# Performance work log

Hardware: AMD Instinct MI355X
Metric: run time of the kernel (lower is better)

The kernel has to match this reference:

```python
import jax, jax.numpy as jnp
import numpy as np

B, C, L = 8, 256, 2048
D = C // 8  # q/k channel dim = 32


def setup_inputs() -> dict:
    key = jax.random.key(0)
    kx, kq, kk, kv, kg = jax.random.split(key, 5)
    kq1, kq2 = jax.random.split(kq)
    kk1, kk2 = jax.random.split(kk)
    kv1, kv2 = jax.random.split(kv)
    s = 0.05
    return {
        "x": jax.random.normal(kx, (B, C, L), dtype=jnp.float32),
        "Wq": jax.random.normal(kq1, (D, C), dtype=jnp.float32) * s,
        "bq": jax.random.normal(kq2, (D,), dtype=jnp.float32) * s,
        "Wk": jax.random.normal(kk1, (D, C), dtype=jnp.float32) * s,
        "bk": jax.random.normal(kk2, (D,), dtype=jnp.float32) * s,
        "Wv": jax.random.normal(kv1, (C, C), dtype=jnp.float32) * s,
        "bv": jax.random.normal(kv2, (C,), dtype=jnp.float32) * s,
        "gamma": jax.random.normal(kg, (1,), dtype=jnp.float32) * 0.1,
    }


def reference(x, Wq, bq, Wk, bk, Wv, bv, gamma):
    # 1x1 Conv1d == per-position channel matmul
    Q = jnp.einsum("dc,bcl->bld", Wq, x) + bq            # (B, L, D)
    K = jnp.einsum("dc,bcl->bdl", Wk, x) + bk[:, None]   # (B, D, L)
    V = jnp.einsum("oc,bcl->bol", Wv, x) + bv[:, None]   # (B, C, L)
    scale = jnp.float32(1.0 / np.sqrt(D))
    # attn[b, i, j]: softmax over j (keys)
    attn = jax.nn.softmax(jnp.einsum("bid,bdj->bij", Q, K) * scale, axis=-1)
    # out = V @ attn^T : out[b, c, i] = sum_j V[b, c, j] * attn[b, i, j]
    out = jnp.einsum("bcj,bij->bci", V, attn)            # (B, C, L)
    return gamma * out + x
```

## Files before the change

### kernel.cpp

```cpp
#include <hip/hip_runtime.h>
#include <stdint.h>


#define BB 8
#define CC 256
#define LL 2048
#define DD 32

typedef unsigned short u16;
typedef __attribute__((ext_vector_type(8))) short short8;
typedef __attribute__((ext_vector_type(4))) float f32x4;

#define SCALE_LOG2E 0.2550348612f

static __device__ __forceinline__ uint32_t pack2bf16(float hi, float lo) {
    return (__float_as_uint(hi) & 0xFFFF0000u) | (__float_as_uint(lo) >> 16);
}

static __device__ __forceinline__ float fexp2(float v) {
#if __has_builtin(__builtin_amdgcn_exp2f)
    return __builtin_amdgcn_exp2f(v);
#else
    return exp2f(v);
#endif
}

static __device__ __forceinline__ float frcp(float v) {
#if __has_builtin(__builtin_amdgcn_rcpf)
    return __builtin_amdgcn_rcpf(v);
#else
    return 1.0f / v;
#endif
}

__global__ __launch_bounds__(256) void prep_w_kernel(
    const float* __restrict__ Wq, const float* __restrict__ Wk,
    const float* __restrict__ Wv, u16* __restrict__ Wh)
{
    int idx = blockIdx.x * 256 + threadIdx.x;
    int r = idx >> 6;
    int c4 = (idx & 63) << 2;
    const float* src;
    if (r < 32)       src = Wq + (size_t)r * CC + c4;
    else if (r < 64)  src = Wk + (size_t)(r - 32) * CC + c4;
    else              src = Wv + (size_t)(r - 64) * CC + c4;
    float4 v = *(const float4*)src;
    uint2 o;
    o.x = pack2bf16(v.y, v.x);
    o.y = pack2bf16(v.w, v.z);
    *(uint2*)(Wh + (size_t)r * CC + c4) = o;
}

__global__ __launch_bounds__(512, 2) void proj_kernel(
    const float* __restrict__ x, const u16* __restrict__ Wh,
    const float* __restrict__ bq, const float* __restrict__ bk,
    const float* __restrict__ bv,
    u16* __restrict__ Qh, u16* __restrict__ Kth, u16* __restrict__ Vh)
{
    __shared__ u16 xls[32 * 264];
    const int blk = blockIdx.x;
    const int b = blk & 7;
    const int l0 = (blk >> 3) << 5;
    const int tid = threadIdx.x;
    const int w = tid >> 6;
    const int lane = tid & 63;
    const int ln = lane & 15;
    const int q = lane >> 4;

#pragma unroll
    for (int cc = 0; cc < 4; ++cc) {
        const int c = cc * 64 + (tid >> 3);
        const int l4 = (tid & 7) * 4;
        const float4 v = *(const float4*)(x + ((size_t)(b * CC + c)) * LL + l0 + l4);
        xls[(l4 + 0) * 264 + c] = (u16)(__float_as_uint(v.x) >> 16);
        xls[(l4 + 1) * 264 + c] = (u16)(__float_as_uint(v.y) >> 16);
        xls[(l4 + 2) * 264 + c] = (u16)(__float_as_uint(v.z) >> 16);
        xls[(l4 + 3) * 264 + c] = (u16)(__float_as_uint(v.w) >> 16);
    }
    __syncthreads();

    const int wl = w & 1;
    const int wm = w >> 1;
    const int mbase = wm * 80;
    const int l = l0 + wl * 16 + ln;

    f32x4 acc[5];
#pragma unroll
    for (int i = 0; i < 5; ++i) acc[i] = (f32x4){0.f, 0.f, 0.f, 0.f};

#pragma unroll
    for (int c0 = 0; c0 < CC; c0 += 32) {
        const short8 bf = *(const short8*)(&xls[(wl * 16 + ln) * 264 + c0 + q * 8]);
#pragma unroll
        for (int mt = 0; mt < 5; ++mt) {
            const short8 af = *(const short8*)(Wh + (size_t)(mbase + mt * 16 + ln) * CC + c0 + q * 8);
            acc[mt] = __builtin_amdgcn_mfma_f32_16x16x32_bf16(af, bf, acc[mt], 0, 0, 0);
        }
    }

#pragma unroll
    for (int mt = 0; mt < 5; ++mt) {
        const int rg = mbase + mt * 16 + q * 4;
        if (rg < 32) {
            float v0 = (acc[mt][0] + bq[rg + 0]) * SCALE_LOG2E;
            float v1 = (acc[mt][1] + bq[rg + 1]) * SCALE_LOG2E;
            float v2 = (acc[mt][2] + bq[rg + 2]) * SCALE_LOG2E;
            float v3 = (acc[mt][3] + bq[rg + 3]) * SCALE_LOG2E;
            uint2 o; o.x = pack2bf16(v1, v0); o.y = pack2bf16(v3, v2);
            *(uint2*)(Qh + ((size_t)(b * LL) + l) * DD + rg) = o;
        } else if (rg < 64) {
            const int rk = rg - 32;
            float v0 = acc[mt][0] + bk[rk + 0];
            float v1 = acc[mt][1] + bk[rk + 1];
            float v2 = acc[mt][2] + bk[rk + 2];
            float v3 = acc[mt][3] + bk[rk + 3];
            uint2 o; o.x = pack2bf16(v1, v0); o.y = pack2bf16(v3, v2);
            *(uint2*)(Kth + ((size_t)(b * LL) + l) * DD + rk) = o;
        } else {
            const int cv = rg - 64;
#pragma unroll
            for (int rr = 0; rr < 4; ++rr) {
                const float v = acc[mt][rr] + bv[cv + rr];
                Vh[((size_t)(b * CC) + cv + rr) * LL + l] = (u16)(__float_as_uint(v) >> 16);
            }
        }
    }
}

#define PJ 136

__global__ __launch_bounds__(512, 4) void attn_kernel(
    const u16* __restrict__ Qh, const u16* __restrict__ Kth,
    const u16* __restrict__ Vh, const float* __restrict__ x,
    const float* __restrict__ gamma, float* __restrict__ out)
{
    __shared__ __attribute__((aligned(16))) u16 pbuf[2][32][PJ];
    __shared__ float lbuf[8][32];

    const int blk = blockIdx.x;
    const int b = blk & 7;
    const int i0 = (blk >> 3) << 5;
    const int tid = threadIdx.x;
    const int w = tid >> 6;
    const int lane = tid & 63;
    const int ln = lane & 15;
    const int q = lane >> 4;

    const u16* Qb = Qh + ((size_t)(b * LL) + i0) * DD;
    const u16* Kb = Kth + ((size_t)(b * LL) + w * 16 + ln) * DD + q * 8;
    const u16* Vb = Vh + ((size_t)(b * CC) + w * 32) * LL;

    short8 qf[2];
#pragma unroll
    for (int it = 0; it < 2; ++it)
        qf[it] = *(const short8*)(Qb + (size_t)(it * 16 + ln) * DD + q * 8);

    const f32x4 zf = {0.f, 0.f, 0.f, 0.f};
    f32x4 oacc[2][2];
#pragma unroll
    for (int a = 0; a < 2; ++a)
#pragma unroll
        for (int c = 0; c < 2; ++c) oacc[a][c] = zf;
    float lsum[2] = {0.f, 0.f};

    short8 kf = *(const short8*)(Kb);

    for (int n = 0; n < 16; ++n) {
        const int jb = n * 128;

        short8 vf[2][4];
#pragma unroll
        for (int ct = 0; ct < 2; ++ct)
#pragma unroll
            for (int kk = 0; kk < 4; ++kk)
                vf[ct][kk] = *(const short8*)(Vb + (size_t)(ct * 16 + ln) * LL + jb + kk * 32 + q * 8);
        const short8 kn = *(const short8*)(Kb + (size_t)((n < 15 ? n + 1 : n) * 128) * DD);

        u16* ps = &pbuf[n & 1][0][0];
#pragma unroll
        for (int it = 0; it < 2; ++it) {
            const f32x4 st = __builtin_amdgcn_mfma_f32_16x16x32_bf16(kf, qf[it], zf, 0, 0, 0);
            const float e0 = fexp2(st[0]), e1 = fexp2(st[1]);
            const float e2 = fexp2(st[2]), e3 = fexp2(st[3]);
            lsum[it] += (e0 + e1) + (e2 + e3);
            uint2 d; d.x = pack2bf16(e1, e0); d.y = pack2bf16(e3, e2);
            *(uint2*)(&ps[(it * 16 + ln) * PJ + w * 16 + q * 4]) = d;
        }
        __syncthreads();

        __builtin_amdgcn_s_setprio(1);
#pragma unroll
        for (int kk = 0; kk < 4; ++kk) {
            const short8 pf0 = *(const short8*)(&ps[(size_t)ln * PJ + kk * 32 + q * 8]);
            const short8 pf1 = *(const short8*)(&ps[(size_t)(16 + ln) * PJ + kk * 32 + q * 8]);
#pragma unroll
            for (int ct = 0; ct < 2; ++ct) {
                oacc[ct][0] = __builtin_amdgcn_mfma_f32_16x16x32_bf16(vf[ct][kk], pf0, oacc[ct][0], 0, 0, 0);
                oacc[ct][1] = __builtin_amdgcn_mfma_f32_16x16x32_bf16(vf[ct][kk], pf1, oacc[ct][1], 0, 0, 0);
            }
        }
        __builtin_amdgcn_s_setprio(0);
        kf = kn;
    }

#pragma unroll
    for (int it = 0; it < 2; ++it) {
        float s = lsum[it];
        s += __shfl_xor(s, 16);
        s += __shfl_xor(s, 32);
        lsum[it] = s;
    }
    if (q == 0) {
        lbuf[w][ln] = lsum[0];
        lbuf[w][16 + ln] = lsum[1];
    }
    __syncthreads();

    float linv[2];
#pragma unroll
    for (int it = 0; it < 2; ++it) {
        float s = 0.f;
#pragma unroll
        for (int w8 = 0; w8 < 8; ++w8) s += lbuf[w8][it * 16 + ln];
        linv[it] = frcp(s);
    }

    const float g = gamma[0];
#pragma unroll
    for (int ct = 0; ct < 2; ++ct)
#pragma unroll
        for (int it = 0; it < 2; ++it) {
#pragma unroll
            for (int r = 0; r < 4; ++r) {
                const int c = w * 32 + ct * 16 + q * 4 + r;
                const size_t idx = ((size_t)(b * CC + c)) * LL + i0 + it * 16 + ln;
                out[idx] = g * (oacc[ct][it][r] * linv[it]) + x[idx];
            }
        }
}

extern "C" void kernel_launch(void* const* d_in, const int* in_sizes, int n_in,
                              void* d_out, int out_size, void* d_ws, size_t ws_size,
                              hipStream_t stream)
{
    const float* x     = (const float*)d_in[0];
    const float* Wq    = (const float*)d_in[1];
    const float* bq    = (const float*)d_in[2];
    const float* Wk    = (const float*)d_in[3];
    const float* bk    = (const float*)d_in[4];
    const float* Wv    = (const float*)d_in[5];
    const float* bv    = (const float*)d_in[6];
    const float* gamma = (const float*)d_in[7];
    float* out = (float*)d_out;

    uint8_t* ws = (uint8_t*)d_ws;
    u16* Wh  = (u16*)(ws + 0x000000);
    u16* Qh  = (u16*)(ws + 0x040000);
    u16* Kth = (u16*)(ws + 0x140000);
    u16* Vh  = (u16*)(ws + 0x240000);

    prep_w_kernel<<<80, 256, 0, stream>>>(Wq, Wk, Wv, Wh);
    proj_kernel<<<512, 512, 0, stream>>>(x, Wh, bq, bk, bv, Qh, Kth, Vh);
    attn_kernel<<<512, 512, 0, stream>>>(Qh, Kth, Vh, x, gamma, out);
}
```

Baseline: 171.0 us.

## Restructure attention tiling per-wave query rows with channel split; stage V stores

The attention kernel is retiled so each block covers 256 query rows and 64 value channels. Each wave owns 32 query rows and computes its own full score rows, which removes the cross-wave P exchange and the row-sum reduction through shared memory. This trades the 8-wave shared softmax tile for recomputing QK^T four times, once per channel group, and halves the grid to 256 blocks with launch bounds of one block per CU. Separately, the projection kernel stages V in LDS so it can be written to global memory with coalesced 16-byte stores instead of scattered 2-byte stores.

```diff
diff --git a/kernel.cpp b/kernel.cpp
--- a/kernel.cpp
+++ b/kernel.cpp
@@ -58,6 +58,7 @@
     u16* __restrict__ Qh, u16* __restrict__ Kth, u16* __restrict__ Vh)
 {
     __shared__ u16 xls[32 * 264];
+    __shared__ __attribute__((aligned(16))) u16 vls[256 * 40];
     const int blk = blockIdx.x;
     const int b = blk & 7;
     const int l0 = (blk >> 3) << 5;
@@ -83,6 +84,7 @@
     const int wm = w >> 1;
     const int mbase = wm * 80;
     const int l = l0 + wl * 16 + ln;
+    const int li = wl * 16 + ln;
 
     f32x4 acc[5];
 #pragma unroll
@@ -121,34 +123,45 @@
 #pragma unroll
             for (int rr = 0; rr < 4; ++rr) {
                 const float v = acc[mt][rr] + bv[cv + rr];
-                Vh[((size_t)(b * CC) + cv + rr) * LL + l] = (u16)(__float_as_uint(v) >> 16);
+                vls[(cv + rr) * 40 + li] = (u16)(__float_as_uint(v) >> 16);
             }
         }
     }
-}
-
-#define PJ 136
-
-__global__ __launch_bounds__(512, 4) void attn_kernel(
+
+    __syncthreads();
+    {
+        const int row = tid >> 1;
+        const int h = (tid & 1) * 16;
+        const u16* src = &vls[row * 40 + h];
+        const uint4 v0 = *(const uint4*)(src);
+        const uint4 v1 = *(const uint4*)(src + 8);
+        uint4* dst = (uint4*)(Vh + ((size_t)(b * CC) + row) * LL + l0 + h);
+        dst[0] = v0;
+        dst[1] = v1;
+    }
+}
+
+__global__ __launch_bounds__(512, 1) void attn_kernel(
     const u16* __restrict__ Qh, const u16* __restrict__ Kth,
     const u16* __restrict__ Vh, const float* __restrict__ x,
     const float* __restrict__ gamma, float* __restrict__ out)
 {
-    __shared__ __attribute__((aligned(16))) u16 pbuf[2][32][PJ];
-    __shared__ float lbuf[8][32];
+    __shared__ __attribute__((aligned(16))) u16 Plds[256][72];
 
     const int blk = blockIdx.x;
-    const int b = blk & 7;
-    const int i0 = (blk >> 3) << 5;
+    const int b  = blk & 7;
+    const int c0 = ((blk >> 3) & 3) << 6;
+    const int i0 = (blk >> 5) << 8;
     const int tid = threadIdx.x;
     const int w = tid >> 6;
     const int lane = tid & 63;
     const int ln = lane & 15;
     const int q = lane >> 4;
 
-    const u16* Qb = Qh + ((size_t)(b * LL) + i0) * DD;
-    const u16* Kb = Kth + ((size_t)(b * LL) + w * 16 + ln) * DD + q * 8;
-    const u16* Vb = Vh + ((size_t)(b * CC) + w * 32) * LL;
+    u16* pb = &Plds[w * 32][0];
+    const u16* Qb = Qh + ((size_t)(b * LL) + i0 + w * 32) * DD;
+    const u16* Kb = Kth + (size_t)(b * LL) * DD;
+    const u16* Vb = Vh + ((size_t)(b * CC) + c0) * LL;
 
     short8 qf[2];
 #pragma unroll
@@ -156,87 +169,86 @@
         qf[it] = *(const short8*)(Qb + (size_t)(it * 16 + ln) * DD + q * 8);
 
     const f32x4 zf = {0.f, 0.f, 0.f, 0.f};
-    f32x4 oacc[2][2];
-#pragma unroll
-    for (int a = 0; a < 2; ++a)
+    f32x4 oacc[4][2];
+#pragma unroll
+    for (int a = 0; a < 4; ++a)
 #pragma unroll
         for (int c = 0; c < 2; ++c) oacc[a][c] = zf;
     float lsum[2] = {0.f, 0.f};
 
-    short8 kf = *(const short8*)(Kb);
-
-    for (int n = 0; n < 16; ++n) {
-        const int jb = n * 128;
-
-        short8 vf[2][4];
-#pragma unroll
-        for (int ct = 0; ct < 2; ++ct)
-#pragma unroll
-            for (int kk = 0; kk < 4; ++kk)
-                vf[ct][kk] = *(const short8*)(Vb + (size_t)(ct * 16 + ln) * LL + jb + kk * 32 + q * 8);
-        const short8 kn = *(const short8*)(Kb + (size_t)((n < 15 ? n + 1 : n) * 128) * DD);
-
-        u16* ps = &pbuf[n & 1][0][0];
-#pragma unroll
-        for (int it = 0; it < 2; ++it) {
-            const f32x4 st = __builtin_amdgcn_mfma_f32_16x16x32_bf16(kf, qf[it], zf, 0, 0, 0);
-            const float e0 = fexp2(st[0]), e1 = fexp2(st[1]);
-            const float e2 = fexp2(st[2]), e3 = fexp2(st[3]);
-            lsum[it] += (e0 + e1) + (e2 + e3);
-            uint2 d; d.x = pack2bf16(e1, e0); d.y = pack2bf16(e3, e2);
-            *(uint2*)(&ps[(it * 16 + ln) * PJ + w * 16 + q * 4]) = d;
-        }
+    short8 kf[4];
+#pragma unroll
+    for (int jt = 0; jt < 4; ++jt)
+        kf[jt] = *(const short8*)(Kb + (size_t)(jt * 16 + ln) * DD + q * 8);
+
+    for (int n = 0; n < 32; ++n) {
+        const int jb = n * 64;
+        const int jbn = (n < 31) ? jb + 64 : jb;
+
+        short8 vf[4][2];
+#pragma unroll
+        for (int ct = 0; ct < 4; ++ct)
+#pragma unroll
+            for (int jk = 0; jk < 2; ++jk)
+                vf[ct][jk] = *(const short8*)(Vb + (size_t)(ct * 16 + ln) * LL + jb + jk * 32 + q * 8);
+        short8 kn[4];
+#pragma unroll
+        for (int jt = 0; jt < 4; ++jt)
+            kn[jt] = *(const short8*)(Kb + (size_t)(jbn + jt * 16 + ln) * DD + q * 8);
+
+#pragma unroll
+        for (int jt = 0; jt < 4; ++jt) {
+#pragma unroll
+            for (int it = 0; it < 2; ++it) {
+                const f32x4 st = __builtin_amdgcn_mfma_f32_16x16x32_bf16(kf[jt], qf[it], zf, 0, 0, 0);
+                const float e0 = fexp2(st[0]), e1 = fexp2(st[1]);
+                const float e2 = fexp2(st[2]), e3 = fexp2(st[3]);
+                lsum[it] += (e0 + e1) + (e2 + e3);
+                uint2 d; d.x = pack2bf16(e1, e0); d.y = pack2bf16(e3, e2);
+                *(uint2*)(&pb[(it * 16 + ln) * 72 + jt * 16 + q * 4]) = d;
+            }
+        }
+
+#pragma unroll
+        for (int jk = 0; jk < 2; ++jk) {
+            short8 pf[2];
+#pragma unroll
+            for (int it = 0; it < 2; ++it)
+                pf[it] = *(const short8*)(&pb[(it * 16 + ln) * 72 + jk * 32 + q * 8]);
+#pragma unroll
+            for (int ct = 0; ct < 4; ++ct)
+#pragma unroll
+                for (int it = 0; it < 2; ++it)
+                    oacc[ct][it] = __builtin_amdgcn_mfma_f32_16x16x32_bf16(
+                        vf[ct][jk], pf[it], oacc[ct][it], 0, 0, 0);
+        }
+
+#pragma unroll
+        for (int jt = 0; jt < 4; ++jt) kf[jt] = kn[jt];
+
         __syncthreads();
-
-        __builtin_amdgcn_s_setprio(1);
-#pragma unroll
-        for (int kk = 0; kk < 4; ++kk) {
-            const short8 pf0 = *(const short8*)(&ps[(size_t)ln * PJ + kk * 32 + q * 8]);
-            const short8 pf1 = *(const short8*)(&ps[(size_t)(16 + ln) * PJ + kk * 32 + q * 8]);
-#pragma unroll
-            for (int ct = 0; ct < 2; ++ct) {
-                oacc[ct][0] = __builtin_amdgcn_mfma_f32_16x16x32_bf16(vf[ct][kk], pf0, oacc[ct][0], 0, 0, 0);
-                oacc[ct][1] = __builtin_amdgcn_mfma_f32_16x16x32_bf16(vf[ct][kk], pf1, oacc[ct][1], 0, 0, 0);
-            }
-        }
-        __builtin_amdgcn_s_setprio(0);
-        kf = kn;
-    }
-
+    }
+
+    float linv[2];
 #pragma unroll
     for (int it = 0; it < 2; ++it) {
         float s = lsum[it];
         s += __shfl_xor(s, 16);
         s += __shfl_xor(s, 32);
-        lsum[it] = s;
-    }
-    if (q == 0) {
-        lbuf[w][ln] = lsum[0];
-        lbuf[w][16 + ln] = lsum[1];
-    }
-    __syncthreads();
-
-    float linv[2];
-#pragma unroll
-    for (int it = 0; it < 2; ++it) {
-        float s = 0.f;
-#pragma unroll
-        for (int w8 = 0; w8 < 8; ++w8) s += lbuf[w8][it * 16 + ln];
         linv[it] = frcp(s);
     }
 
     const float g = gamma[0];
 #pragma unroll
-    for (int ct = 0; ct < 2; ++ct)
-#pragma unroll
-        for (int it = 0; it < 2; ++it) {
+    for (int ct = 0; ct < 4; ++ct)
+#pragma unroll
+        for (int it = 0; it < 2; ++it)
 #pragma unroll
             for (int r = 0; r < 4; ++r) {
-                const int c = w * 32 + ct * 16 + q * 4 + r;
-                const size_t idx = ((size_t)(b * CC + c)) * LL + i0 + it * 16 + ln;
+                const int c = c0 + ct * 16 + q * 4 + r;
+                const size_t idx = ((size_t)(b * CC + c)) * LL + i0 + w * 32 + it * 16 + ln;
                 out[idx] = g * (oacc[ct][it][r] * linv[it]) + x[idx];
             }
-        }
 }
 
 extern "C" void kernel_launch(void* const* d_in, const int* in_sizes, int n_in,
@@ -261,5 +273,5 @@
 
     prep_w_kernel<<<80, 256, 0, stream>>>(Wq, Wk, Wv, Wh);
     proj_kernel<<<512, 512, 0, stream>>>(x, Wh, bq, bk, bv, Qh, Kth, Vh);
-    attn_kernel<<<512, 512, 0, stream>>>(Qh, Kth, Vh, x, gamma, out);
-}
+    attn_kernel<<<256, 512, 0, stream>>>(Qh, Kth, Vh, x, gamma, out);
+}
```

After: 180.6 us. 5.6% more time.
